# Kernel optimization log

Hardware: AMD Instinct MI355X
Metric: run time of the kernel (lower is better)

## Reference

```python
import jax, jax.numpy as jnp
import numpy as np

NUM_HEADS = 16

def setup_inputs() -> dict:
    key = jax.random.key(0)
    ks = jax.random.split(key, 5)
    d_model = 1024
    x = jax.random.normal(ks[0], (2, 2048, d_model), dtype=jnp.float32)
    # xavier-uniform-like scale for square [d_model, d_model] weights
    lim = float(np.sqrt(6.0 / (d_model + d_model)))
    def w(k):
        return jax.random.uniform(k, (d_model, d_model), dtype=jnp.float32, minval=-lim, maxval=lim)
    return {"x": x, "Wq": w(ks[1]), "Wk": w(ks[2]), "Wv": w(ks[3]), "Wo": w(ks[4])}

def reference(x, Wq, Wk, Wv, Wo):
    B, S, D = x.shape
    H = NUM_HEADS
    dk = D // H
    # project: torch does x @ W.T
    def split_heads(t):
        return t.reshape(B, S, H, dk).transpose(0, 2, 1, 3)  # [B,H,S,dk]
    q = split_heads(x @ Wq.T)
    k = split_heads(x @ Wk.T)
    v = split_heads(x @ Wv.T)
    scores = jnp.einsum('bhqd,bhkd->bhqk', q, k) / jnp.sqrt(jnp.float32(dk))
    causal = jnp.tril(jnp.ones((S, S), dtype=bool))  # True where attended
    scores = jnp.where(causal[None, None], scores, -jnp.inf)
    probs = jax.nn.softmax(scores, axis=-1)
    out = jnp.einsum('bhqk,bhkd->bhqd', probs, v)  # [B,H,S,dk]
    out = out.transpose(0, 2, 1, 3).reshape(B, S, D)
    return out @ Wo.T
```

## Files before the change

### kernel.cpp

```cpp
#include <hip/hip_runtime.h>
#include <stdint.h>

#define BATCH  2
#define SEQ    2048
#define DMODEL 1024
#define NHEADS 16
#define DKH    64
#define MTOT   (BATCH*SEQ)
#define VSTR   (SEQ + 32)

typedef unsigned short u16;
typedef __bf16 bf16x8 __attribute__((ext_vector_type(8)));
typedef float  f32x4  __attribute__((ext_vector_type(4)));

extern "C" __device__ float __ocml_native_exp2_f32(float);

__device__ __forceinline__ u16 f2bf(float f) {
  union { float f; uint32_t u; } v; v.f = f;
  uint32_t u = v.u;
  return (u16)((u + 0x7FFFu + ((u >> 16) & 1u)) >> 16);
}
__device__ __forceinline__ float bf2f(u16 h) {
  union { uint32_t u; float f; } v; v.u = (uint32_t)h << 16; return v.f;
}

__device__ __forceinline__ void gld_lds16(const void* g, void* l) {
  __builtin_amdgcn_global_load_lds(
      (__attribute__((address_space(1))) void*)g,
      (__attribute__((address_space(3))) void*)l, 16, 0, 0);
}

__device__ __forceinline__ uint32_t cvtpk(float lo, float hi) {
  uint32_t r;
  asm("v_cvt_pk_bf16_f32 %0, %1, %2" : "=v"(r) : "v"(lo), "v"(hi));
  return r;
}
__device__ __forceinline__ void pl16swap(uint32_t& a, uint32_t& b) {
  asm volatile("v_permlane16_swap_b32 %0, %1" : "+v"(a), "+v"(b));
}

__global__ void cvt_f32_bf16(const float* __restrict__ src, u16* __restrict__ dst) {
  size_t i = ((size_t)blockIdx.x * 256 + threadIdx.x) * 4;
  float4 f = *(const float4*)(src + i);
  ushort4 o;
  o.x = f2bf(f.x); o.y = f2bf(f.y); o.z = f2bf(f.z); o.w = f2bf(f.w);
  *(ushort4*)(dst + i) = o;
}
__global__ void cvt_w(const float* __restrict__ a, const float* __restrict__ b,
                      const float* __restrict__ c, const float* __restrict__ d,
                      u16* __restrict__ dst) {
  const float* srcs[4] = {a, b, c, d};
  const float* s = srcs[blockIdx.y];
  size_t i = ((size_t)blockIdx.x * 256 + threadIdx.x) * 4;
  float4 f = *(const float4*)(s + i);
  ushort4 o;
  o.x = f2bf(f.x); o.y = f2bf(f.y); o.z = f2bf(f.z); o.w = f2bf(f.w);
  *(ushort4*)(dst + (size_t)blockIdx.y * (DMODEL*DMODEL) + i) = o;
}

__global__ __launch_bounds__(256, 3) void gemm_qkv(
    const u16* __restrict__ xb, const u16* __restrict__ wq,
    const u16* __restrict__ wk, const u16* __restrict__ wv,
    u16* __restrict__ q, u16* __restrict__ k, u16* __restrict__ v, float qscale) {
  __shared__ __align__(16) u16 lA[128 * 64];
  __shared__ __align__(16) u16 lB[3][64 * 64];

  const int tid  = threadIdx.x;
  const int lane = tid & 63;
  const int lrow = lane & 15;
  const int quad = lane >> 4;
  const int wave = tid >> 6;
  const int wm   = (wave & 1) * 64;
  const int wn   = (wave >> 1) * 32;
  const int sx   = lrow & 7;
  const int m0 = blockIdx.x * 128, n0 = blockIdx.y * 64;
  const u16* Ws[3] = {wq, wk, wv};

  f32x4 acc[3][4][2] = {};

  for (int k0 = 0; k0 < DMODEL; k0 += 64) {
    #pragma unroll
    for (int r = 0; r < 4; ++r) {
      int off  = r * 4096 + tid * 16;
      int row  = off >> 7;
      int c16  = (off >> 4) & 7;
      int colb = (c16 ^ (row & 7)) << 4;
      gld_lds16((const char*)xb + ((size_t)(m0 + row) * DMODEL + k0) * 2 + colb,
                (char*)lA + off);
    }
    #pragma unroll
    for (int z = 0; z < 3; ++z)
      #pragma unroll
      for (int r = 0; r < 2; ++r) {
        int off  = r * 4096 + tid * 16;
        int row  = off >> 7;
        int c16  = (off >> 4) & 7;
        int colb = (c16 ^ (row & 7)) << 4;
        gld_lds16((const char*)Ws[z] + ((size_t)(n0 + row) * DMODEL + k0) * 2 + colb,
                  (char*)&lB[z][0] + off);
      }
    __syncthreads();
    #pragma unroll
    for (int ks = 0; ks < 2; ++ks) {
      const int ro = ((((ks << 2) | quad) ^ sx) << 3);
      bf16x8 a[4], b[3][2];
      #pragma unroll
      for (int i = 0; i < 4; ++i)
        a[i] = *(const bf16x8*)(lA + (wm + i*16 + lrow) * 64 + ro);
      #pragma unroll
      for (int z = 0; z < 3; ++z)
        #pragma unroll
        for (int j = 0; j < 2; ++j)
          b[z][j] = *(const bf16x8*)(&lB[z][0] + (wn + j*16 + lrow) * 64 + ro);
      #pragma unroll
      for (int z = 0; z < 3; ++z)
        #pragma unroll
        for (int i = 0; i < 4; ++i)
          #pragma unroll
          for (int j = 0; j < 2; ++j)
            acc[z][i][j] = __builtin_amdgcn_mfma_f32_16x16x32_bf16(a[i], b[z][j], acc[z][i][j], 0, 0, 0);
    }
    __syncthreads();
  }

  const int rb = quad * 4, cb = lrow;
  const int h  = blockIdx.y;
  u16* outs[3] = {q, k, v};
  #pragma unroll
  for (int z = 0; z < 3; ++z) {
    u16* out = outs[z];
    if (z == 2) {
      #pragma unroll
      for (int i = 0; i < 4; ++i)
        #pragma unroll
        for (int j = 0; j < 2; ++j) {
          int row0 = m0 + wm + i*16 + rb;
          int d_   = wn + j*16 + cb;
          int b_ = row0 >> 11, s0 = row0 & 2047;
          ushort4 pk;
          pk.x = f2bf(acc[z][i][j][0]); pk.y = f2bf(acc[z][i][j][1]);
          pk.z = f2bf(acc[z][i][j][2]); pk.w = f2bf(acc[z][i][j][3]);
          *(ushort4*)&out[((size_t)(b_*NHEADS + h) * DKH + d_) * VSTR + s0] = pk;
        }
    } else {
      const float scale = (z == 0) ? qscale : 1.0f;
      #pragma unroll
      for (int i = 0; i < 4; ++i)
        #pragma unroll
        for (int j = 0; j < 2; ++j)
          #pragma unroll
          for (int r = 0; r < 4; ++r) {
            int row = m0 + wm + i*16 + rb + r;
            int d_  = wn + j*16 + cb;
            int b_ = row >> 11, s_ = row & 2047;
            out[(((size_t)(b_*NHEADS + h) * SEQ + s_) << 6) + d_] =
                f2bf(acc[z][i][j][r] * scale);
          }
    }
  }
}

__device__ __forceinline__ void gemm_core64(const u16* A, const u16* W,
                                            int m0, int n0, f32x4 acc[4][2],
                                            u16* lA, u16* lB) {
  const int tid  = threadIdx.x;
  const int lane = tid & 63;
  const int lrow = lane & 15;
  const int quad = lane >> 4;
  const int wave = tid >> 6;
  const int wm   = (wave & 1) * 64;
  const int wn   = (wave >> 1) * 32;
  const int sx   = lrow & 7;

  for (int k0 = 0; k0 < DMODEL; k0 += 64) {
    #pragma unroll
    for (int r = 0; r < 4; ++r) {
      int off  = r * 4096 + tid * 16;
      int row  = off >> 7;
      int c16  = (off >> 4) & 7;
      int colb = (c16 ^ (row & 7)) << 4;
      gld_lds16((const char*)A + ((size_t)(m0 + row) * DMODEL + k0) * 2 + colb,
                (char*)lA + off);
    }
    #pragma unroll
    for (int r = 0; r < 2; ++r) {
      int off  = r * 4096 + tid * 16;
      int row  = off >> 7;
      int c16  = (off >> 4) & 7;
      int colb = (c16 ^ (row & 7)) << 4;
      gld_lds16((const char*)W + ((size_t)(n0 + row) * DMODEL + k0) * 2 + colb,
                (char*)lB + off);
    }
    __syncthreads();
    #pragma unroll
    for (int ks = 0; ks < 2; ++ks) {
      bf16x8 a[4], b[2];
      const int ro = ((((ks << 2) | quad) ^ sx) << 3);
      #pragma unroll
      for (int i = 0; i < 4; ++i)
        a[i] = *(const bf16x8*)(lA + (wm + i*16 + lrow) * 64 + ro);
      #pragma unroll
      for (int j = 0; j < 2; ++j)
        b[j] = *(const bf16x8*)(lB + (wn + j*16 + lrow) * 64 + ro);
      #pragma unroll
      for (int i = 0; i < 4; ++i)
        #pragma unroll
        for (int j = 0; j < 2; ++j)
          acc[i][j] = __builtin_amdgcn_mfma_f32_16x16x32_bf16(a[i], b[j], acc[i][j], 0, 0, 0);
    }
    __syncthreads();
  }
}

__global__ __launch_bounds__(256, 3) void gemm_out(
    const u16* __restrict__ ab, const u16* __restrict__ wo, float* __restrict__ out) {
  __shared__ __align__(16) u16 lA[128 * 64];
  __shared__ __align__(16) u16 lB[64 * 64];
  const int m0 = blockIdx.x * 128, n0 = blockIdx.y * 64;
  f32x4 acc[4][2] = {};
  gemm_core64(ab, wo, m0, n0, acc, lA, lB);

  const int lane = threadIdx.x & 63;
  const int wave = threadIdx.x >> 6;
  const int wm = (wave & 1) * 64, wn = (wave >> 1) * 32;
  const int rb = (lane >> 4) * 4, cb = lane & 15;
  #pragma unroll
  for (int i = 0; i < 4; ++i)
    #pragma unroll
    for (int j = 0; j < 2; ++j)
      #pragma unroll
      for (int r = 0; r < 4; ++r)
        out[(size_t)(m0 + wm + i*16 + rb + r) * DMODEL + (n0 + wn + j*16 + cb)]
            = acc[i][j][r];
}

__device__ const uint8_t JT[40] = {
  60,61,62,63, 56,57,58, 52,53,54, 48,49,50, 44,45,46, 40,41, 36,37,
  32,33, 28,29, 24, 20, 16, 12,
  59,42,25,8, 55,38,21,4, 51,34,17,0
};

__device__ __forceinline__ void stage_kv(const u16* Kg, const u16* Vg, int t,
                                         u16* lK, u16* lV, int tid) {
  #pragma unroll
  for (int r = 0; r < 2; ++r) {
    int off  = r * 4096 + tid * 16;
    int row  = off >> 7;
    int colb = (((off >> 4) & 7) ^ (row & 7)) << 4;
    gld_lds16((const char*)Kg + ((size_t)(t*64 + row) * DKH) * 2 + colb,
              (char*)lK + off);
    gld_lds16((const char*)Vg + ((size_t)row * VSTR + t*64) * 2 + colb,
              (char*)lV + off);
  }
}

__global__ __launch_bounds__(256, 2) void attn(
    const u16* __restrict__ Q, const u16* __restrict__ K,
    const u16* __restrict__ V, u16* __restrict__ O,
    u16* __restrict__ po, float* __restrict__ pl) {
  __shared__ __align__(16) u16 lK[2][64 * 64];
  __shared__ __align__(16) u16 lV[2][64 * 64];

  const int tid  = threadIdx.x;
  const int wid  = tid >> 6;
  const int lane = tid & 63;
  const int lrow = lane & 15;
  const int quad = lane >> 4;
  const int sx   = lrow & 7;
  const int pq   = ((quad & 1) << 1) | (quad >> 1);

  const int g  = blockIdx.x >> 5;
  const int bh = blockIdx.x & 31;
  const int e  = JT[g];
  const int u  = e >> 2, c = e & 3;
  const int lo = c * 8;
  const int T  = 2*u + 2;
  const int hi = (lo + 8 < T) ? lo + 8 : T;
  const int td = 2*u + (wid >> 1);
  const int qg0 = 128*u + 32*wid;

  const u16* Qg = Q + (size_t)bh * SEQ * DKH;
  const u16* Kg = K + (size_t)bh * SEQ * DKH;
  const u16* Vg = V + (size_t)bh * DKH * VSTR;

  bf16x8 aq[2][2];
  #pragma unroll
  for (int i = 0; i < 2; ++i)
    #pragma unroll
    for (int ks = 0; ks < 2; ++ks)
      aq[i][ks] = *(const bf16x8*)(Qg + (size_t)(qg0 + 16*i + lrow) * DKH + ks*32 + quad*8);

  f32x4 o_acc[2][4] = {};
  float l_acc[2] = {};

  stage_kv(Kg, Vg, lo, &lK[0][0], &lV[0][0], tid);
  __syncthreads();
  int cur = 0;

  for (int t = lo; t < hi; ++t) {
    if (t + 1 < hi)
      stage_kv(Kg, Vg, t + 1, &lK[cur ^ 1][0], &lV[cur ^ 1][0], tid);

    bf16x8 kf[2][4], vf[2][4];
    #pragma unroll
    for (int ks = 0; ks < 2; ++ks) {
      const int kro = ((((ks << 2) | quad) ^ sx) << 3);
      const int vro = ((((ks << 2) | pq)   ^ sx) << 3);
      #pragma unroll
      for (int j = 0; j < 4; ++j) {
        kf[ks][j] = *(const bf16x8*)(&lK[cur][0] + (j*16 + lrow) * 64 + kro);
        vf[ks][j] = *(const bf16x8*)(&lV[cur][0] + (j*16 + lrow) * 64 + vro);
      }
    }

    #pragma unroll
    for (int i = 0; i < 2; ++i) {
      f32x4 s_acc[4] = {};
      #pragma unroll
      for (int ks = 0; ks < 2; ++ks)
        #pragma unroll
        for (int j = 0; j < 4; ++j)
          s_acc[j] = __builtin_amdgcn_mfma_f32_16x16x32_bf16(kf[ks][j], aq[i][ks], s_acc[j], 0, 0, 0);

      if (t >= td) {
        const int qrel = qg0 + 16*i + lrow - 64*t;
        #pragma unroll
        for (int j = 0; j < 4; ++j) {
          int kl = j*16 + quad*4;
          #pragma unroll
          for (int r = 0; r < 4; ++r)
            if (kl + r > qrel) s_acc[j][r] = -1e30f;
        }
      }

      uint32_t w[4][2];
      float ls = 0.f;
      #pragma unroll
      for (int j = 0; j < 4; ++j) {
        float p0 = __ocml_native_exp2_f32(s_acc[j][0]);
        float p1 = __ocml_native_exp2_f32(s_acc[j][1]);
        float p2 = __ocml_native_exp2_f32(s_acc[j][2]);
        float p3 = __ocml_native_exp2_f32(s_acc[j][3]);
        ls += (p0 + p1) + (p2 + p3);
        w[j][0] = cvtpk(p0, p1);
        w[j][1] = cvtpk(p2, p3);
      }
      l_acc[i] += ls;

      pl16swap(w[0][0], w[1][0]);
      pl16swap(w[0][1], w[1][1]);
      pl16swap(w[2][0], w[3][0]);
      pl16swap(w[2][1], w[3][1]);
      union { uint32_t u[4]; bf16x8 v; } g0, g1;
      g0.u[0] = w[0][0]; g0.u[1] = w[0][1]; g0.u[2] = w[1][0]; g0.u[3] = w[1][1];
      g1.u[0] = w[2][0]; g1.u[1] = w[2][1]; g1.u[2] = w[3][0]; g1.u[3] = w[3][1];

      #pragma unroll
      for (int j = 0; j < 4; ++j)
        o_acc[i][j] = __builtin_amdgcn_mfma_f32_16x16x32_bf16(g0.v, vf[0][j], o_acc[i][j], 0, 0, 0);
      #pragma unroll
      for (int j = 0; j < 4; ++j)
        o_acc[i][j] = __builtin_amdgcn_mfma_f32_16x16x32_bf16(g1.v, vf[1][j], o_acc[i][j], 0, 0, 0);
    }

    __syncthreads();
    cur ^= 1;
  }

  float lr[2][4];
  #pragma unroll
  for (int i = 0; i < 2; ++i) {
    float s = l_acc[i];
    s += __shfl_xor(s, 16, 64);
    s += __shfl_xor(s, 32, 64);
    #pragma unroll
    for (int r = 0; r < 4; ++r)
      lr[i][r] = __shfl(s, quad*4 + r, 16);
  }

  if (T <= 8) {
    const int h = bh & 15, b_ = bh >> 4;
    #pragma unroll
    for (int i = 0; i < 2; ++i)
      #pragma unroll
      for (int j = 0; j < 4; ++j)
        #pragma unroll
        for (int r = 0; r < 4; ++r) {
          int sg = qg0 + 16*i + quad*4 + r;
          O[(size_t)(b_ * SEQ + sg) * DMODEL + h * DKH + j*16 + lrow]
              = f2bf(o_acc[i][j][r] / lr[i][r]);
        }
  } else {
    const int pold = td;
    const int base = (pold < 16) ? (pold - 8) * 2
                   : (pold < 24) ? 16 + (pold - 16) * 3
                   :               40 + (pold - 24) * 4;
    const int slot = (base + c) * 32 + bh;
    const int r64  = 32 * (wid & 1);
    #pragma unroll
    for (int i = 0; i < 2; ++i) {
      #pragma unroll
      for (int j = 0; j < 4; ++j) {
        ushort4 pk;
        pk.x = f2bf(o_acc[i][j][0]); pk.y = f2bf(o_acc[i][j][1]);
        pk.z = f2bf(o_acc[i][j][2]); pk.w = f2bf(o_acc[i][j][3]);
        *(ushort4*)&po[(size_t)slot * 4096 + (j*16 + lrow) * 64 + r64 + 16*i + quad*4] = pk;
      }
      if (lrow == 0)
        #pragma unroll
        for (int r = 0; r < 4; ++r)
          pl[slot * 64 + r64 + 16*i + quad*4 + r] = lr[i][r];
    }
  }
}

__global__ __launch_bounds__(256) void combine(
    const u16* __restrict__ po, const float* __restrict__ pl, u16* __restrict__ ab) {
  __shared__ u16 Ls[64][68];
  const int b  = blockIdx.x;
  const int p  = 8 + (b >> 5);
  const int bh = b & 31;
  const int t  = threadIdx.x;
  const int col = t >> 2;
  const int r0  = (t & 3) * 16;
  const int base = (p < 16) ? (p - 8) * 2
                 : (p < 24) ? 16 + (p - 16) * 3
                 :            40 + (p - 24) * 4;
  const int nc   = (p < 16) ? 2 : (p < 24) ? 3 : 4;

  float acc[16], lsum[16];
  const size_t s0 = (size_t)(base * 32 + bh);
  const u16*   q0 = po + s0 * 4096 + col * 64 + r0;
  const float* l0 = pl + s0 * 64 + r0;
  #pragma unroll
  for (int q4 = 0; q4 < 4; ++q4) {
    ushort4 a  = *(const ushort4*)(q0 + q4 * 4);
    ushort4 c2 = *(const ushort4*)(q0 + (size_t)32 * 4096 + q4 * 4);
    acc[q4*4+0] = bf2f(a.x) + bf2f(c2.x);
    acc[q4*4+1] = bf2f(a.y) + bf2f(c2.y);
    acc[q4*4+2] = bf2f(a.z) + bf2f(c2.z);
    acc[q4*4+3] = bf2f(a.w) + bf2f(c2.w);
    float4 f = *(const float4*)(l0 + q4 * 4);
    float4 g = *(const float4*)(l0 + 32 * 64 + q4 * 4);
    lsum[q4*4+0] = f.x + g.x; lsum[q4*4+1] = f.y + g.y;
    lsum[q4*4+2] = f.z + g.z; lsum[q4*4+3] = f.w + g.w;
  }
  if (nc >= 3) {
    #pragma unroll
    for (int q4 = 0; q4 < 4; ++q4) {
      ushort4 a = *(const ushort4*)(q0 + (size_t)64 * 4096 + q4 * 4);
      acc[q4*4+0] += bf2f(a.x); acc[q4*4+1] += bf2f(a.y);
      acc[q4*4+2] += bf2f(a.z); acc[q4*4+3] += bf2f(a.w);
      float4 f = *(const float4*)(l0 + 64 * 64 + q4 * 4);
      lsum[q4*4+0] += f.x; lsum[q4*4+1] += f.y;
      lsum[q4*4+2] += f.z; lsum[q4*4+3] += f.w;
    }
  }
  if (nc == 4) {
    #pragma unroll
    for (int q4 = 0; q4 < 4; ++q4) {
      ushort4 a = *(const ushort4*)(q0 + (size_t)96 * 4096 + q4 * 4);
      acc[q4*4+0] += bf2f(a.x); acc[q4*4+1] += bf2f(a.y);
      acc[q4*4+2] += bf2f(a.z); acc[q4*4+3] += bf2f(a.w);
      float4 f = *(const float4*)(l0 + 96 * 64 + q4 * 4);
      lsum[q4*4+0] += f.x; lsum[q4*4+1] += f.y;
      lsum[q4*4+2] += f.z; lsum[q4*4+3] += f.w;
    }
  }
  #pragma unroll
  for (int q = 0; q < 16; ++q)
    Ls[r0 + q][col] = f2bf(acc[q] / lsum[q]);
  __syncthreads();

  const int row = t >> 2;
  const int c0  = (t & 3) * 16;
  const int b_ = bh >> 4, h = bh & 15;
  u16* dst = ab + (size_t)(b_ * SEQ + 64 * p + row) * DMODEL + h * DKH + c0;
  #pragma unroll
  for (int q = 0; q < 16; q += 4)
    *(ushort4*)(dst + q) = *(const ushort4*)&Ls[row][c0 + q];
}

extern "C" void kernel_launch(void* const* d_in, const int* in_sizes, int n_in,
                              void* d_out, int out_size, void* d_ws, size_t ws_size,
                              hipStream_t stream) {
  const float* x  = (const float*)d_in[0];
  const float* Wq = (const float*)d_in[1];
  const float* Wk = (const float*)d_in[2];
  const float* Wv = (const float*)d_in[3];
  const float* Wo = (const float*)d_in[4];
  float* out = (float*)d_out;

  u16* xb  = (u16*)d_ws;
  u16* wqb = xb  + (size_t)MTOT * DMODEL;
  u16* wkb = wqb + (size_t)DMODEL * DMODEL;
  u16* wvb = wkb + (size_t)DMODEL * DMODEL;
  u16* wob = wvb + (size_t)DMODEL * DMODEL;
  u16* qb  = wob + (size_t)DMODEL * DMODEL;
  u16* kb  = qb  + (size_t)MTOT * DMODEL;
  u16* vb  = kb  + (size_t)MTOT * DMODEL;
  u16* ab  = vb  + (size_t)BATCH * NHEADS * DKH * VSTR;
  u16* po  = ab  + (size_t)MTOT * DMODEL;
  float* pl = (float*)(po + (size_t)2304 * 4096);

  cvt_f32_bf16<<<MTOT * DMODEL / 1024, 256, 0, stream>>>(x, xb);
  cvt_w<<<dim3(DMODEL * DMODEL / 1024, 4), 256, 0, stream>>>(Wq, Wk, Wv, Wo, wqb);

  const float qscale = 0.125f * 1.44269504088896340736f;
  gemm_qkv<<<dim3(32, 16), 256, 0, stream>>>(
      xb, wqb, wkb, wvb, qb, kb, vb, qscale);

  attn<<<1280, 256, 0, stream>>>(qb, kb, vb, ab, po, pl);
  combine<<<768, 256, 0, stream>>>(po, pl, ab);

  gemm_out<<<dim3(32, 16), 256, 0, stream>>>(ab, wob, out);
}
```

Measured before the change: 164.3 us.

## Split K/V fragment loads, batch QK MFMAs, raise occupancy, add setprio

Raises the launch-bounds occupancy hint from 2 to 3 waves per SIMD. The loop now loads only the K fragments first and issues all QK^T MFMAs for both query sub-tiles together. V fragments are loaded afterwards, which shortens the K fragments' register lifetime. MFMA bursts are wrapped in s_setprio so waves in their matrix phase get issue priority over waves doing exp and softmax. The tighter register budget may force spills, and holding both score tiles at once adds register pressure.

```diff
diff --git a/kernel.cpp b/kernel.cpp
--- a/kernel.cpp
+++ b/kernel.cpp
@@ -254,7 +254,7 @@
   }
 }
 
-__global__ __launch_bounds__(256, 2) void attn(
+__global__ __launch_bounds__(256, 3) void attn(
     const u16* __restrict__ Q, const u16* __restrict__ K,
     const u16* __restrict__ V, u16* __restrict__ O,
     u16* __restrict__ po, float* __restrict__ pl) {
@@ -301,27 +301,38 @@
     if (t + 1 < hi)
       stage_kv(Kg, Vg, t + 1, &lK[cur ^ 1][0], &lV[cur ^ 1][0], tid);
 
-    bf16x8 kf[2][4], vf[2][4];
+    f32x4 s_acc[2][4] = {};
+    {
+      bf16x8 kf[2][4];
+      #pragma unroll
+      for (int ks = 0; ks < 2; ++ks) {
+        const int kro = ((((ks << 2) | quad) ^ sx) << 3);
+        #pragma unroll
+        for (int j = 0; j < 4; ++j)
+          kf[ks][j] = *(const bf16x8*)(&lK[cur][0] + (j*16 + lrow) * 64 + kro);
+      }
+      __builtin_amdgcn_s_setprio(1);
+      #pragma unroll
+      for (int i = 0; i < 2; ++i)
+        #pragma unroll
+        for (int ks = 0; ks < 2; ++ks)
+          #pragma unroll
+          for (int j = 0; j < 4; ++j)
+            s_acc[i][j] = __builtin_amdgcn_mfma_f32_16x16x32_bf16(kf[ks][j], aq[i][ks], s_acc[i][j], 0, 0, 0);
+      __builtin_amdgcn_s_setprio(0);
+    }
+
+    bf16x8 vf[2][4];
     #pragma unroll
     for (int ks = 0; ks < 2; ++ks) {
-      const int kro = ((((ks << 2) | quad) ^ sx) << 3);
-      const int vro = ((((ks << 2) | pq)   ^ sx) << 3);
-      #pragma unroll
-      for (int j = 0; j < 4; ++j) {
-        kf[ks][j] = *(const bf16x8*)(&lK[cur][0] + (j*16 + lrow) * 64 + kro);
+      const int vro = ((((ks << 2) | pq) ^ sx) << 3);
+      #pragma unroll
+      for (int j = 0; j < 4; ++j)
         vf[ks][j] = *(const bf16x8*)(&lV[cur][0] + (j*16 + lrow) * 64 + vro);
-      }
     }
 
     #pragma unroll
     for (int i = 0; i < 2; ++i) {
-      f32x4 s_acc[4] = {};
-      #pragma unroll
-      for (int ks = 0; ks < 2; ++ks)
-        #pragma unroll
-        for (int j = 0; j < 4; ++j)
-          s_acc[j] = __builtin_amdgcn_mfma_f32_16x16x32_bf16(kf[ks][j], aq[i][ks], s_acc[j], 0, 0, 0);
-
       if (t >= td) {
         const int qrel = qg0 + 16*i + lrow - 64*t;
         #pragma unroll
@@ -329,7 +340,7 @@
           int kl = j*16 + quad*4;
           #pragma unroll
           for (int r = 0; r < 4; ++r)
-            if (kl + r > qrel) s_acc[j][r] = -1e30f;
+            if (kl + r > qrel) s_acc[i][j][r] = -1e30f;
         }
       }
 
@@ -337,10 +348,10 @@
       float ls = 0.f;
       #pragma unroll
       for (int j = 0; j < 4; ++j) {
-        float p0 = __ocml_native_exp2_f32(s_acc[j][0]);
-        float p1 = __ocml_native_exp2_f32(s_acc[j][1]);
-        float p2 = __ocml_native_exp2_f32(s_acc[j][2]);
-        float p3 = __ocml_native_exp2_f32(s_acc[j][3]);
+        float p0 = __ocml_native_exp2_f32(s_acc[i][j][0]);
+        float p1 = __ocml_native_exp2_f32(s_acc[i][j][1]);
+        float p2 = __ocml_native_exp2_f32(s_acc[i][j][2]);
+        float p3 = __ocml_native_exp2_f32(s_acc[i][j][3]);
         ls += (p0 + p1) + (p2 + p3);
         w[j][0] = cvtpk(p0, p1);
         w[j][1] = cvtpk(p2, p3);
@@ -355,12 +366,14 @@
       g0.u[0] = w[0][0]; g0.u[1] = w[0][1]; g0.u[2] = w[1][0]; g0.u[3] = w[1][1];
       g1.u[0] = w[2][0]; g1.u[1] = w[2][1]; g1.u[2] = w[3][0]; g1.u[3] = w[3][1];
 
+      __builtin_amdgcn_s_setprio(1);
       #pragma unroll
       for (int j = 0; j < 4; ++j)
         o_acc[i][j] = __builtin_amdgcn_mfma_f32_16x16x32_bf16(g0.v, vf[0][j], o_acc[i][j], 0, 0, 0);
       #pragma unroll
       for (int j = 0; j < 4; ++j)
         o_acc[i][j] = __builtin_amdgcn_mfma_f32_16x16x32_bf16(g1.v, vf[1][j], o_acc[i][j], 0, 0, 0);
+      __builtin_amdgcn_s_setprio(0);
     }
 
     __syncthreads();
```

After: 163.1 us. About the same (-0.7%).
